# Optimization experiments

Measured on AMD Instinct MI355X. Metric: run time of the kernel, lower is better.

## Reference

```python
import jax, jax.numpy as jnp
import numpy as np

T = 0.07
TOPK = 5

def _l2norm(x, axis=-1, eps=1e-12):
    n = jnp.sqrt(jnp.sum(x * x, axis=axis, keepdims=True))
    return x / jnp.maximum(n, eps)

def setup_inputs() -> dict:
    key = jax.random.key(0)
    k1, k2, k3, k4, k5 = jax.random.split(key, 5)
    b, nc, dim, dim_mlp, K = 256, 5, 128, 2048, 65536
    q = jax.random.normal(k1, (b, nc, dim), jnp.float32)
    k = jax.random.normal(k2, (b, dim), jnp.float32)
    q_backbone = jax.random.normal(k3, (b, nc, dim_mlp), jnp.float32)
    # queues are column-normalized buffers, as in __init__
    queue = _l2norm(jax.random.normal(k4, (dim, K), jnp.float32), axis=0)
    queue_backbone = _l2norm(jax.random.normal(k5, (dim_mlp, K), jnp.float32), axis=0)
    return {"q": q, "k": k, "q_backbone": q_backbone,
            "queue": queue, "queue_backbone": queue_backbone}

def reference(q, k, q_backbone, queue, queue_backbone):
    b, nc, dim = q.shape
    dim_mlp = q_backbone.shape[-1]
    qn = _l2norm(q)                 # [b, nc, dim]
    kn = _l2norm(k)                 # [b, dim]
    qb = _l2norm(q_backbone)        # [b, nc, dim_mlp]

    # positive logits: each crop vs its key
    l_pos = jnp.einsum('bnd,bd->bn', qn, kn).reshape(-1, 1)      # [b*nc, 1]
    # negative logits vs queue
    l_neg = jnp.einsum('nc,ck->nk', qn.reshape(-1, dim), queue)  # [b*nc, K]
    logits = jnp.concatenate([l_pos, l_neg], axis=1) / T
    labels = jnp.zeros((logits.shape[0],), dtype=jnp.int32)

    # backbone-space similarities to pick top-k neighbors
    l_neg_backbone = jnp.einsum('nc,ck->nk', qb.reshape(-1, dim_mlp), queue_backbone)

    # pull_topk: softmax CE pulling toward top-k backbone neighbors.
    # scatter-mask + masked mean == gather log-softmax at top-k indices (indices distinct)
    _, knn_idx = jax.lax.top_k(l_neg_backbone, TOPK)             # [b*nc, TOPK]
    log_prob = jax.nn.log_softmax(l_neg / T, axis=1)             # [b*nc, K]
    pos_logp = jnp.take_along_axis(log_prob, knn_idx, axis=1)    # [b*nc, TOPK]
    loss = -jnp.mean(jnp.mean(pos_logp, axis=1))
    return logits, labels, loss
```

## Files before the change

### kernel.cpp

```cpp
#include <hip/hip_runtime.h>
#include <hip/hip_bf16.h>

#define M_     1280
#define DIM    128
#define DMLP   2048
#define KQ     65536
#define NCOLS  65537ull
#define NTOPK  5
#define NCHUNK 256
#define NBLK1  512
#define NTK    32
#define INV_T  14.285714285714286f

typedef __attribute__((ext_vector_type(8))) short bf16x8;
typedef __attribute__((ext_vector_type(4))) float f32x4;

static __device__ __forceinline__ unsigned short f2bf(float x){
  union { __hip_bfloat16 h; unsigned short u; } cv;
  cv.h = __float2bfloat16(x);
  return cv.u;
}

#define GLDS16(gp, lp) __builtin_amdgcn_global_load_lds( \
    (const __attribute__((address_space(1))) void*)(gp), \
    (__attribute__((address_space(3))) void*)(lp), 16, 0, 0)

#define BAR()   asm volatile("s_barrier" ::: "memory")
#define VMW(n)  asm volatile("s_waitcnt vmcnt(" #n ")" ::: "memory")

__global__ __launch_bounds__(256) void transpose_bf16(
    const float* __restrict__ in, unsigned short* __restrict__ out, int R, int C){
  __shared__ float tile[64][65];
  const int c0 = blockIdx.x * 64, r0 = blockIdx.y * 64;
  const int t = threadIdx.x;
  #pragma unroll
  for (int i = 0; i < 4; ++i){
    int lin = t + i * 256;
    int rr = lin >> 4;
    int cc = (lin & 15) * 4;
    const float4 v = *(const float4*)(in + (size_t)(r0 + rr) * C + c0 + cc);
    tile[rr][cc + 0] = v.x; tile[rr][cc + 1] = v.y;
    tile[rr][cc + 2] = v.z; tile[rr][cc + 3] = v.w;
  }
  __syncthreads();
  #pragma unroll
  for (int i = 0; i < 4; ++i){
    int lin = t + i * 256;
    int oc  = lin >> 4;
    int orr = (lin & 15) * 4;
    ushort4 u;
    u.x = f2bf(tile[orr + 0][oc]); u.y = f2bf(tile[orr + 1][oc]);
    u.z = f2bf(tile[orr + 2][oc]); u.w = f2bf(tile[orr + 3][oc]);
    *(ushort4*)(out + (size_t)(c0 + oc) * R + r0 + orr) = u;
  }
}

__global__ __launch_bounds__(128) void normq_kernel(
    const float* __restrict__ q, const float* __restrict__ k,
    unsigned short* __restrict__ qn, float* __restrict__ outp){
  const int i = blockIdx.x;
  const int t = threadIdx.x;
  const float qv = q[(size_t)i * DIM + t];
  const float kv = k[(size_t)(i / 5) * DIM + t];
  float a = qv * qv, b = kv * kv, d = qv * kv;
  #pragma unroll
  for (int s = 32; s >= 1; s >>= 1){
    a += __shfl_down(a, s, 64);
    b += __shfl_down(b, s, 64);
    d += __shfl_down(d, s, 64);
  }
  __shared__ float red[6];
  if ((t & 63) == 0){ red[(t >> 6) * 3 + 0] = a; red[(t >> 6) * 3 + 1] = b; red[(t >> 6) * 3 + 2] = d; }
  __syncthreads();
  const float qq = red[0] + red[3], kk = red[1] + red[4], qk = red[2] + red[5];
  const float qnorm = fmaxf(sqrtf(qq), 1e-12f);
  qn[(size_t)i * DIM + t] = f2bf(qv / qnorm);
  if (t == 0){
    const float knorm = fmaxf(sqrtf(kk), 1e-12f);
    outp[(size_t)i * NCOLS] = (qk / (qnorm * knorm)) * INV_T;
  }
}

__global__ __launch_bounds__(256) void normqb_kernel(
    const float* __restrict__ qb, unsigned short* __restrict__ out){
  const int i = blockIdx.x, t = threadIdx.x;
  const float* p = qb + (size_t)i * DMLP;
  float x[8]; float ss = 0.f;
  #pragma unroll
  for (int j = 0; j < 8; ++j){ x[j] = p[t + j * 256]; ss += x[j] * x[j]; }
  #pragma unroll
  for (int s = 32; s >= 1; s >>= 1) ss += __shfl_down(ss, s, 64);
  __shared__ float r4[4];
  if ((t & 63) == 0) r4[t >> 6] = ss;
  __syncthreads();
  const float tot = r4[0] + r4[1] + r4[2] + r4[3];
  const float inv = 1.0f / fmaxf(sqrtf(tot), 1e-12f);
  unsigned short* o = out + (size_t)i * DMLP;
  #pragma unroll
  for (int j = 0; j < 8; ++j) o[t + j * 256] = f2bf(x[j] * inv);
}

static __device__ __forceinline__ void tk_insert(float* v, int* ix, float nv, int ni){
  if (nv > v[4]){
    v[4] = nv; ix[4] = ni;
    #pragma unroll
    for (int j = 4; j > 0; --j){
      if (v[j] > v[j - 1]){
        float tv = v[j]; v[j] = v[j - 1]; v[j - 1] = tv;
        int   ti = ix[j]; ix[j] = ix[j - 1]; ix[j - 1] = ti;
      }
    }
  }
}

__global__ __launch_bounds__(256) void gemm1_mfma(
    const unsigned short* __restrict__ A, const unsigned short* __restrict__ BT,
    float* __restrict__ outp, float* __restrict__ pm, float* __restrict__ ps){
  __shared__ __attribute__((aligned(16))) unsigned char smem[16512];
  unsigned short* At = (unsigned short*)smem;
  unsigned short* Bt = At + 128 * 32;

  const int t    = threadIdx.x;
  const int lane = t & 63;
  const int wv   = t >> 6;
  const int lid  = lane & 15;
  const int quad = lane >> 4;
  const int m0 = blockIdx.x * 128;
  const int n0 = blockIdx.y * 128;

  f32x4 acc[2][8];
  #pragma unroll
  for (int mt = 0; mt < 2; ++mt)
    #pragma unroll
    for (int nt = 0; nt < 8; ++nt)
      acc[mt][nt] = f32x4{0.f, 0.f, 0.f, 0.f};

  const int arow = t >> 2;
  const int ace  = (t & 3) * 8;

  for (int kt = 0; kt < DIM; kt += 32){
    if (kt) __syncthreads();
    #pragma unroll
    for (int it = 0; it < 2; ++it){
      int row = arow + it * 64;
      GLDS16(A  + (size_t)(m0 + row) * DIM + kt + ace, At + (t + it * 256) * 8);
    }
    #pragma unroll
    for (int it = 0; it < 2; ++it){
      int row = arow + it * 64;
      GLDS16(BT + (size_t)(n0 + row) * DIM + kt + ace, Bt + (t + it * 256) * 8);
    }
    asm volatile("s_waitcnt vmcnt(0)" ::: "memory");
    __syncthreads();

    bf16x8 af[2], bfr[8];
    #pragma unroll
    for (int mt = 0; mt < 2; ++mt)
      af[mt] = *(const bf16x8*)(At + (wv * 32 + mt * 16 + lid) * 32 + quad * 8);
    #pragma unroll
    for (int nt = 0; nt < 8; ++nt)
      bfr[nt] = *(const bf16x8*)(Bt + (nt * 16 + lid) * 32 + quad * 8);
    #pragma unroll
    for (int mt = 0; mt < 2; ++mt)
      #pragma unroll
      for (int nt = 0; nt < 8; ++nt)
        acc[mt][nt] = __builtin_amdgcn_mfma_f32_16x16x32_bf16(af[mt], bfr[nt], acc[mt][nt], 0, 0, 0);
  }

  float mx[2][4], sm[2][4];
  #pragma unroll
  for (int mt = 0; mt < 2; ++mt)
    #pragma unroll
    for (int r = 0; r < 4; ++r) mx[mt][r] = -3.0e38f;
  #pragma unroll
  for (int mt = 0; mt < 2; ++mt)
    #pragma unroll
    for (int nt = 0; nt < 8; ++nt)
      #pragma unroll
      for (int r = 0; r < 4; ++r){
        const int mg = m0 + wv * 32 + mt * 16 + quad * 4 + r;
        const int ng = n0 + nt * 16 + lid;
        const float x = acc[mt][nt][r] * INV_T;
        outp[(size_t)mg * NCOLS + 1 + ng] = x;
        mx[mt][r] = fmaxf(mx[mt][r], x);
      }
  #pragma unroll
  for (int mt = 0; mt < 2; ++mt)
    #pragma unroll
    for (int r = 0; r < 4; ++r){
      #pragma unroll
      for (int s = 8; s >= 1; s >>= 1)
        mx[mt][r] = fmaxf(mx[mt][r], __shfl_xor(mx[mt][r], s, 64));
      sm[mt][r] = 0.f;
    }
  #pragma unroll
  for (int mt = 0; mt < 2; ++mt)
    #pragma unroll
    for (int nt = 0; nt < 8; ++nt)
      #pragma unroll
      for (int r = 0; r < 4; ++r)
        sm[mt][r] += __expf(acc[mt][nt][r] * INV_T - mx[mt][r]);
  #pragma unroll
  for (int mt = 0; mt < 2; ++mt)
    #pragma unroll
    for (int r = 0; r < 4; ++r){
      #pragma unroll
      for (int s = 8; s >= 1; s >>= 1)
        sm[mt][r] += __shfl_xor(sm[mt][r], s, 64);
      if (lid == 0){
        const int mg = m0 + wv * 32 + mt * 16 + quad * 4 + r;
        pm[(size_t)mg * NBLK1 + blockIdx.y] = mx[mt][r];
        ps[(size_t)mg * NBLK1 + blockIdx.y] = sm[mt][r];
      }
    }
}


static __device__ __forceinline__ void stage_half_g2_dummy(){}

#define RDA(mi_, SRC) do { _Pragma("unroll") for (int mf = 0; mf < 4; ++mf){ \
    const int R_ = (mi_) * 128 + wm * 64 + mf * 16 + lid; \
    av[mi_][mf][0] = *(const bf16x8*)((SRC) + R_ * 64 + sw0); \
    av[mi_][mf][1] = *(const bf16x8*)((SRC) + R_ * 64 + sw1); } } while(0)

#define RDB(nj_, SRC) do { _Pragma("unroll") for (int nf = 0; nf < 2; ++nf){ \
    const int S_ = (nj_) * 128 + wn * 32 + nf * 16 + lid; \
    bv[nj_][nf][0] = *(const bf16x8*)((SRC) + S_ * 64 + sw0); \
    bv[nj_][nf][1] = *(const bf16x8*)((SRC) + S_ * 64 + sw1); } } while(0)

#define MMQ(mi_, nj_) do { __builtin_amdgcn_s_setprio(1); \
    _Pragma("unroll") for (int mf = 0; mf < 4; ++mf) \
    _Pragma("unroll") for (int nf = 0; nf < 2; ++nf){ \
      acc[mi_][nj_][mf][nf] = __builtin_amdgcn_mfma_f32_16x16x32_bf16(av[mi_][mf][0], bv[nj_][nf][0], acc[mi_][nj_][mf][nf], 0, 0, 0); \
      acc[mi_][nj_][mf][nf] = __builtin_amdgcn_mfma_f32_16x16x32_bf16(av[mi_][mf][1], bv[nj_][nf][1], acc[mi_][nj_][mf][nf], 0, 0, 0); } \
    __builtin_amdgcn_s_setprio(0); } while(0)

#define STAGE(base, kc, dst) do { \
  GLDS16((base) + ro0 + (kc), (dst) + t * 8); \
  GLDS16((base) + ro1 + (kc), (dst) + (512 + t) * 8); } while(0)

__global__ __launch_bounds__(512, 2) void gemm2_topk(
    const unsigned short* __restrict__ A, const unsigned short* __restrict__ BT,
    float* __restrict__ cval, int* __restrict__ cidx){
  __shared__ __attribute__((aligned(16))) unsigned short lds[2][2][256 * 64];

  const int t    = threadIdx.x;
  const int lane = t & 63;
  const int wv   = t >> 6;
  const int wm   = wv >> 2;
  const int wn   = wv & 3;
  const int lid  = lane & 15;
  const int quad = lane >> 4;
  const int l7   = lid & 7;
  const int sw0  = ((quad    ) ^ l7) * 8;
  const int sw1  = ((quad ^ 4) ^ l7) * 8;

  const int h  = blockIdx.x;
  const int wg = (h & 7) * 160 + (h >> 3);
  const int bm = wg % 5;
  const int bn = wg / 5;
  const int m0 = bm * 256;
  const int n0 = bn * 256;

  const int r0s = t >> 3,        r1s = (512 + t) >> 3;
  const int g0  = (t & 7) ^ (r0s & 7), g1 = (t & 7) ^ (r1s & 7);
  const int ro0 = r0s * DMLP + g0 * 8;
  const int ro1 = r1s * DMLP + g1 * 8;
  const unsigned short* aB0 = A  + (size_t)m0          * DMLP;
  const unsigned short* aB1 = A  + (size_t)(m0 + 128)  * DMLP;
  const unsigned short* bB0 = BT + (size_t)n0          * DMLP;
  const unsigned short* bB1 = BT + (size_t)(n0 + 128)  * DMLP;

  f32x4 acc[2][2][4][2];
  #pragma unroll
  for (int a = 0; a < 2; ++a)
    #pragma unroll
    for (int b = 0; b < 2; ++b)
      #pragma unroll
      for (int c = 0; c < 4; ++c)
        #pragma unroll
        for (int d = 0; d < 2; ++d)
          acc[a][b][c][d] = f32x4{0.f, 0.f, 0.f, 0.f};

  bf16x8 av[2][4][2];
  bf16x8 bv[2][2][2];

  STAGE(aB0, 0, &lds[0][0][0]);
  STAGE(bB0, 0, &lds[0][1][0]);
  STAGE(aB1, 0, &lds[0][0][128 * 64]);
  STAGE(bB1, 0, &lds[0][1][128 * 64]);
  VMW(0);
  BAR();

  #pragma unroll 2
  for (int kt = 0; kt < NTK; ++kt){
    unsigned short* curA = &lds[kt & 1][0][0];
    unsigned short* curB = &lds[kt & 1][1][0];
    unsigned short* nxtA = &lds[(kt + 1) & 1][0][0];
    unsigned short* nxtB = &lds[(kt + 1) & 1][1][0];

    if (kt) MMQ(0, 1);

    RDA(0, curA);
    RDB(0, curB);

    if (kt + 1 < NTK){
      const int kc = (kt + 1) * 64;
      STAGE(aB0, kc, nxtA);
      STAGE(bB0, kc, nxtB);
      STAGE(aB1, kc, nxtA + 128 * 64);
      STAGE(bB1, kc, nxtB + 128 * 64);
    }

    MMQ(0, 0);
    RDA(1, curA);
    MMQ(1, 0);
    RDB(1, curB);
    MMQ(1, 1);

    VMW(0);
    BAR();
  }
  MMQ(0, 1);

  float* scratch = (float*)&lds[0][0][0];
  const int erow = t >> 2;
  const int eh   = t & 3;
  #pragma unroll
  for (int mi = 0; mi < 2; ++mi){
    float v[5]; int ix[5];
    #pragma unroll
    for (int j = 0; j < 5; ++j){ v[j] = -3.0e38f; ix[j] = 0; }
    #pragma unroll
    for (int nj = 0; nj < 2; ++nj){
      __syncthreads();
      #pragma unroll
      for (int mf = 0; mf < 4; ++mf)
        #pragma unroll
        for (int nf = 0; nf < 2; ++nf)
          #pragma unroll
          for (int r = 0; r < 4; ++r)
            scratch[(wm * 64 + mf * 16 + quad * 4 + r) * 133 + wn * 32 + nf * 16 + lid]
              = acc[mi][nj][mf][nf][r];
      __syncthreads();
      for (int j = 0; j < 32; ++j)
        tk_insert(v, ix, scratch[erow * 133 + j * 4 + eh], n0 + nj * 128 + j * 4 + eh);
    }
    #pragma unroll
    for (int s = 1; s <= 2; s <<= 1){
      float pv[5]; int pi[5];
      #pragma unroll
      for (int j = 0; j < 5; ++j){ pv[j] = __shfl_xor(v[j], s, 64); pi[j] = __shfl_xor(ix[j], s, 64); }
      #pragma unroll
      for (int j = 0; j < 5; ++j) tk_insert(v, ix, pv[j], pi[j]);
    }
    if (eh == 0){
      const int rowg = m0 + mi * 128 + erow;
      const size_t cb = ((size_t)rowg * NCHUNK + bn) * NTOPK;
      #pragma unroll
      for (int j = 0; j < 5; ++j){ cval[cb + j] = v[j]; cidx[cb + j] = ix[j]; }
    }
  }
}

__global__ __launch_bounds__(256) void topk_merge(
    const float* __restrict__ cval, const int* __restrict__ cidx, int* __restrict__ knn){
  const int row = blockIdx.x, t = threadIdx.x;
  float v[5]; int ix[5];
  #pragma unroll
  for (int j = 0; j < 5; ++j){ v[j] = -3.0e38f; ix[j] = 0; }
  const size_t base = (size_t)row * (NCHUNK * NTOPK);
  #pragma unroll
  for (int j = 0; j < 5; ++j){
    const int c = t * 5 + j;
    tk_insert(v, ix, cval[base + c], cidx[base + c]);
  }
  __shared__ float lv[256 * 5];
  __shared__ int   li[256 * 5];
  #pragma unroll
  for (int j = 0; j < 5; ++j){ lv[t * 5 + j] = v[j]; li[t * 5 + j] = ix[j]; }
  __syncthreads();
  if (t < 64){
    float v2[5]; int ix2[5];
    #pragma unroll
    for (int j = 0; j < 5; ++j){ v2[j] = -3.0e38f; ix2[j] = 0; }
    for (int L = 0; L < 4; ++L)
      #pragma unroll
      for (int j = 0; j < 5; ++j)
        tk_insert(v2, ix2, lv[(t * 4 + L) * 5 + j], li[(t * 4 + L) * 5 + j]);
    #pragma unroll
    for (int s = 32; s >= 1; s >>= 1){
      float pv[5]; int pi[5];
      #pragma unroll
      for (int j = 0; j < 5; ++j){ pv[j] = __shfl_down(v2[j], s, 64); pi[j] = __shfl_down(ix2[j], s, 64); }
      #pragma unroll
      for (int j = 0; j < 5; ++j) tk_insert(v2, ix2, pv[j], pi[j]);
    }
    if (t == 0){
      #pragma unroll
      for (int j = 0; j < 5; ++j) knn[(size_t)row * NTOPK + j] = ix2[j];
    }
  }
}

__global__ __launch_bounds__(256) void lse_merge(
    const float* __restrict__ pm, const float* __restrict__ ps,
    float* __restrict__ lse){
  const int row = blockIdx.x, t = threadIdx.x;
  const float* pmr = pm + (size_t)row * NBLK1;
  const float* psr = ps + (size_t)row * NBLK1;
  float m = -1.0e30f, s = 0.f;
  #pragma unroll
  for (int c = 0; c < 2; ++c){
    const float om = pmr[t + c * 256], os = psr[t + c * 256];
    const float nm = fmaxf(m, om);
    s = s * __expf(m - nm) + os * __expf(om - nm);
    m = nm;
  }
  #pragma unroll
  for (int sh = 32; sh >= 1; sh >>= 1){
    const float om = __shfl_down(m, sh, 64), os = __shfl_down(s, sh, 64);
    const float nm = fmaxf(m, om);
    s = s * __expf(m - nm) + os * __expf(om - nm);
    m = nm;
  }
  __shared__ float sm2[4], ss2[4];
  if ((t & 63) == 0){ sm2[t >> 6] = m; ss2[t >> 6] = s; }
  __syncthreads();
  if (t == 0){
    float M = sm2[0], S = ss2[0];
    #pragma unroll
    for (int w = 1; w < 4; ++w){
      const float nm = fmaxf(M, sm2[w]);
      S = S * __expf(M - nm) + ss2[w] * __expf(sm2[w] - nm);
      M = nm;
    }
    lse[row] = M + __logf(S);
  }
}

__global__ __launch_bounds__(256) void loss_kernel(
    const float* __restrict__ logits, const float* __restrict__ lse,
    const int* __restrict__ knn, float* __restrict__ loss){
  const int i = blockIdx.x * 256 + threadIdx.x;
  float c = 0.f;
  if (i < M_){
    const float l = lse[i];
    #pragma unroll
    for (int j = 0; j < 5; ++j){
      const int id = knn[(size_t)i * NTOPK + j];
      c += l - logits[(size_t)i * NCOLS + 1 + id];
    }
    c *= (1.0f / 6400.0f);
  }
  #pragma unroll
  for (int s = 32; s >= 1; s >>= 1) c += __shfl_down(c, s, 64);
  if ((threadIdx.x & 63) == 0) atomicAdd(loss, c);
}

extern "C" void kernel_launch(void* const* d_in, const int* in_sizes, int n_in,
                              void* d_out, int out_size, void* d_ws, size_t ws_size,
                              hipStream_t stream){
  const float* q   = (const float*)d_in[0];
  const float* k   = (const float*)d_in[1];
  const float* qbI = (const float*)d_in[2];
  const float* que = (const float*)d_in[3];
  const float* qbb = (const float*)d_in[4];
  float* out = (float*)d_out;

  unsigned char* w = (unsigned char*)d_ws;
  unsigned short* qn   = (unsigned short*)w; w += (size_t)M_ * DIM  * 2;
  unsigned short* qbn  = (unsigned short*)w; w += (size_t)M_ * DMLP * 2;
  unsigned short* queT = (unsigned short*)w; w += (size_t)KQ * DIM  * 2;
  unsigned short* qbbT = (unsigned short*)w; w += (size_t)KQ * DMLP * 2;
  float* cval = (float*)w;                   w += (size_t)M_ * NCHUNK * NTOPK * 4;
  int*   cidx = (int*)w;                     w += (size_t)M_ * NCHUNK * NTOPK * 4;
  int*   knn  = (int*)w;                     w += (size_t)M_ * NTOPK * 4;
  float* lseb = (float*)w;                   w += (size_t)M_ * 4;
  float* pm   = (float*)w;                   w += (size_t)M_ * NBLK1 * 4;
  float* ps   = (float*)w;                   w += (size_t)M_ * NBLK1 * 4;

  hipMemsetAsync(out + (size_t)M_ * NCOLS, 0, (M_ + 1) * sizeof(float), stream);

  transpose_bf16<<<dim3(KQ / 64, DIM  / 64), 256, 0, stream>>>(que, queT, DIM,  KQ);
  transpose_bf16<<<dim3(KQ / 64, DMLP / 64), 256, 0, stream>>>(qbb, qbbT, DMLP, KQ);
  normq_kernel <<<M_, 128, 0, stream>>>(q, k, qn, out);
  normqb_kernel<<<M_, 256, 0, stream>>>(qbI, qbn);
  gemm1_mfma<<<dim3(10, NBLK1), 256, 0, stream>>>(qn, queT, out, pm, ps);
  gemm2_topk<<<dim3(1280), 512, 0, stream>>>(qbn, qbbT, cval, cidx);
  topk_merge<<<M_, 256, 0, stream>>>(cval, cidx, knn);
  lse_merge<<<M_, 256, 0, stream>>>(pm, ps, lseb);
  loss_kernel<<<(M_ + 255) / 256, 256, 0, stream>>>(out, lseb, knn,
                                                    out + (size_t)M_ * NCOLS + M_);
}
```

Before: 1.386 ms.

## Run backbone top-k GEMM in FP8 e4m3 with a repacked LDS layout

The backbone queue transpose and the normalized backbone queries are now quantized to FP8 e4m3 instead of bf16. The top-k GEMM kernel is rewritten around 16x16x32 fp8 MFMA, with a new swizzled 64-byte-row LDS layout and a smaller shared buffer so launch bounds allow 4 blocks per CU. This halves global and LDS bytes for the largest GEMM and the transpose writes. The cost is much coarser precision: normalized 2048-d vectors have entries near the e4m3 subnormal range, so the top-5 neighbor indices may differ from the reference.

```diff
diff --git a/kernel.cpp b/kernel.cpp
--- a/kernel.cpp
+++ b/kernel.cpp
@@ -1,5 +1,6 @@
 #include <hip/hip_runtime.h>
 #include <hip/hip_bf16.h>
+#include <hip/hip_fp8.h>
 
 #define M_     1280
 #define DIM    128
@@ -21,6 +22,11 @@
   return cv.u;
 }
 
+static __device__ __forceinline__ unsigned char f2f8(float x){
+  __hip_fp8_e4m3 h(x);
+  return (unsigned char)h.__x;
+}
+
 #define GLDS16(gp, lp) __builtin_amdgcn_global_load_lds( \
     (const __attribute__((address_space(1))) void*)(gp), \
     (__attribute__((address_space(3))) void*)(lp), 16, 0, 0)
@@ -52,6 +58,33 @@
     u.x = f2bf(tile[orr + 0][oc]); u.y = f2bf(tile[orr + 1][oc]);
     u.z = f2bf(tile[orr + 2][oc]); u.w = f2bf(tile[orr + 3][oc]);
     *(ushort4*)(out + (size_t)(c0 + oc) * R + r0 + orr) = u;
+  }
+}
+
+__global__ __launch_bounds__(256) void transpose_fp8(
+    const float* __restrict__ in, unsigned char* __restrict__ out, int R, int C){
+  __shared__ float tile[64][65];
+  const int c0 = blockIdx.x * 64, r0 = blockIdx.y * 64;
+  const int t = threadIdx.x;
+  #pragma unroll
+  for (int i = 0; i < 4; ++i){
+    int lin = t + i * 256;
+    int rr = lin >> 4;
+    int cc = (lin & 15) * 4;
+    const float4 v = *(const float4*)(in + (size_t)(r0 + rr) * C + c0 + cc);
+    tile[rr][cc + 0] = v.x; tile[rr][cc + 1] = v.y;
+    tile[rr][cc + 2] = v.z; tile[rr][cc + 3] = v.w;
+  }
+  __syncthreads();
+  #pragma unroll
+  for (int i = 0; i < 4; ++i){
+    int lin = t + i * 256;
+    int oc  = lin >> 4;
+    int orr = (lin & 15) * 4;
+    uchar4 u;
+    u.x = f2f8(tile[orr + 0][oc]); u.y = f2f8(tile[orr + 1][oc]);
+    u.z = f2f8(tile[orr + 2][oc]); u.w = f2f8(tile[orr + 3][oc]);
+    *(uchar4*)(out + (size_t)(c0 + oc) * R + r0 + orr) = u;
   }
 }
 
@@ -82,7 +115,7 @@
 }
 
 __global__ __launch_bounds__(256) void normqb_kernel(
-    const float* __restrict__ qb, unsigned short* __restrict__ out){
+    const float* __restrict__ qb, unsigned char* __restrict__ out){
   const int i = blockIdx.x, t = threadIdx.x;
   const float* p = qb + (size_t)i * DMLP;
   float x[8]; float ss = 0.f;
@@ -95,9 +128,9 @@
   __syncthreads();
   const float tot = r4[0] + r4[1] + r4[2] + r4[3];
   const float inv = 1.0f / fmaxf(sqrtf(tot), 1e-12f);
-  unsigned short* o = out + (size_t)i * DMLP;
-  #pragma unroll
-  for (int j = 0; j < 8; ++j) o[t + j * 256] = f2bf(x[j] * inv);
+  unsigned char* o = out + (size_t)i * DMLP;
+  #pragma unroll
+  for (int j = 0; j < 8; ++j) o[t + j * 256] = f2f8(x[j] * inv);
 }
 
 static __device__ __forceinline__ void tk_insert(float* v, int* ix, float nv, int ni){
@@ -216,33 +249,29 @@
 }
 
 
-static __device__ __forceinline__ void stage_half_g2_dummy(){}
-
-#define RDA(mi_, SRC) do { _Pragma("unroll") for (int mf = 0; mf < 4; ++mf){ \
-    const int R_ = (mi_) * 128 + wm * 64 + mf * 16 + lid; \
-    av[mi_][mf][0] = *(const bf16x8*)((SRC) + R_ * 64 + sw0); \
-    av[mi_][mf][1] = *(const bf16x8*)((SRC) + R_ * 64 + sw1); } } while(0)
-
-#define RDB(nj_, SRC) do { _Pragma("unroll") for (int nf = 0; nf < 2; ++nf){ \
-    const int S_ = (nj_) * 128 + wn * 32 + nf * 16 + lid; \
-    bv[nj_][nf][0] = *(const bf16x8*)((SRC) + S_ * 64 + sw0); \
-    bv[nj_][nf][1] = *(const bf16x8*)((SRC) + S_ * 64 + sw1); } } while(0)
-
-#define MMQ(mi_, nj_) do { __builtin_amdgcn_s_setprio(1); \
+#define RDA8(mi_, SRC) do { _Pragma("unroll") for (int mf = 0; mf < 4; ++mf){ \
+    const int rr = ((mi_) * 64 + wm * 32 + mf * 8 + r2l) * 128; \
+    av[mi_][mf][0] = *(const long*)((SRC) + rr + c0f); \
+    av[mi_][mf][1] = *(const long*)((SRC) + rr + c1f); } } while(0)
+
+#define RDB8(nj_, SRC) do { _Pragma("unroll") for (int nf = 0; nf < 2; ++nf){ \
+    const int rr = ((nj_) * 64 + wn * 16 + nf * 8 + r2l) * 128; \
+    bv[nf][0] = *(const long*)((SRC) + rr + c0f); \
+    bv[nf][1] = *(const long*)((SRC) + rr + c1f); } } while(0)
+
+#define MMQ8(mi_, nj_) do { __builtin_amdgcn_s_setprio(1); \
     _Pragma("unroll") for (int mf = 0; mf < 4; ++mf) \
     _Pragma("unroll") for (int nf = 0; nf < 2; ++nf){ \
-      acc[mi_][nj_][mf][nf] = __builtin_amdgcn_mfma_f32_16x16x32_bf16(av[mi_][mf][0], bv[nj_][nf][0], acc[mi_][nj_][mf][nf], 0, 0, 0); \
-      acc[mi_][nj_][mf][nf] = __builtin_amdgcn_mfma_f32_16x16x32_bf16(av[mi_][mf][1], bv[nj_][nf][1], acc[mi_][nj_][mf][nf], 0, 0, 0); } \
+      acc[mi_][nj_][mf][nf] = __builtin_amdgcn_mfma_f32_16x16x32_fp8_fp8(av[mi_][mf][0], bv[nf][0], acc[mi_][nj_][mf][nf], 0, 0, 0); \
+      acc[mi_][nj_][mf][nf] = __builtin_amdgcn_mfma_f32_16x16x32_fp8_fp8(av[mi_][mf][1], bv[nf][1], acc[mi_][nj_][mf][nf], 0, 0, 0); } \
     __builtin_amdgcn_s_setprio(0); } while(0)
 
-#define STAGE(base, kc, dst) do { \
-  GLDS16((base) + ro0 + (kc), (dst) + t * 8); \
-  GLDS16((base) + ro1 + (kc), (dst) + (512 + t) * 8); } while(0)
-
-__global__ __launch_bounds__(512, 2) void gemm2_topk(
-    const unsigned short* __restrict__ A, const unsigned short* __restrict__ BT,
+#define STAGE8(base, kc, dst) GLDS16((base) + roff + (kc), (dst) + (size_t)t * 16)
+
+__global__ __launch_bounds__(512, 4) void gemm2_topk(
+    const unsigned char* __restrict__ A, const unsigned char* __restrict__ BT,
     float* __restrict__ cval, int* __restrict__ cidx){
-  __shared__ __attribute__((aligned(16))) unsigned short lds[2][2][256 * 64];
+  __shared__ __attribute__((aligned(16))) unsigned char smem[66048];
 
   const int t    = threadIdx.x;
   const int lane = t & 63;
@@ -251,9 +280,9 @@
   const int wn   = wv & 3;
   const int lid  = lane & 15;
   const int quad = lane >> 4;
-  const int l7   = lid & 7;
-  const int sw0  = ((quad    ) ^ l7) * 8;
-  const int sw1  = ((quad ^ 4) ^ l7) * 8;
+  const int r2l  = lid >> 1;
+  const int c0f = ((((lid & 1) * 4 + 0 + (quad >> 1)) ^ r2l) * 16) + (quad & 1) * 8;
+  const int c1f = ((((lid & 1) * 4 + 2 + (quad >> 1)) ^ r2l) * 16) + (quad & 1) * 8;
 
   const int h  = blockIdx.x;
   const int wg = (h & 7) * 160 + (h >> 3);
@@ -262,14 +291,15 @@
   const int m0 = bm * 256;
   const int n0 = bn * 256;
 
-  const int r0s = t >> 3,        r1s = (512 + t) >> 3;
-  const int g0  = (t & 7) ^ (r0s & 7), g1 = (t & 7) ^ (r1s & 7);
-  const int ro0 = r0s * DMLP + g0 * 8;
-  const int ro1 = r1s * DMLP + g1 * 8;
-  const unsigned short* aB0 = A  + (size_t)m0          * DMLP;
-  const unsigned short* aB1 = A  + (size_t)(m0 + 128)  * DMLP;
-  const unsigned short* bB0 = BT + (size_t)n0          * DMLP;
-  const unsigned short* bB1 = BT + (size_t)(n0 + 128)  * DMLP;
+  const int p     = t;
+  const int r2loc = p >> 3;
+  const int u     = (p & 7) ^ (r2loc & 7);
+  const int rloc  = r2loc * 2 + (u >> 2);
+  const size_t roff = (size_t)rloc * DMLP + (u & 3) * 16;
+  const unsigned char* aB0 = A  + (size_t)m0 * DMLP;
+  const unsigned char* aB1 = A  + (size_t)(m0 + 128) * DMLP;
+  const unsigned char* bB0 = BT + (size_t)n0 * DMLP;
+  const unsigned char* bB1 = BT + (size_t)(n0 + 128) * DMLP;
 
   f32x4 acc[2][2][4][2];
   #pragma unroll
@@ -282,48 +312,48 @@
         for (int d = 0; d < 2; ++d)
           acc[a][b][c][d] = f32x4{0.f, 0.f, 0.f, 0.f};
 
-  bf16x8 av[2][4][2];
-  bf16x8 bv[2][2][2];
-
-  STAGE(aB0, 0, &lds[0][0][0]);
-  STAGE(bB0, 0, &lds[0][1][0]);
-  STAGE(aB1, 0, &lds[0][0][128 * 64]);
-  STAGE(bB1, 0, &lds[0][1][128 * 64]);
+  long av[2][4][2];
+  long bv[2][2];
+
+  STAGE8(aB0, 0, smem);
+  STAGE8(bB0, 0, smem + 16384);
+  STAGE8(aB1, 0, smem + 8192);
+  STAGE8(bB1, 0, smem + 16384 + 8192);
   VMW(0);
   BAR();
 
   #pragma unroll 2
   for (int kt = 0; kt < NTK; ++kt){
-    unsigned short* curA = &lds[kt & 1][0][0];
-    unsigned short* curB = &lds[kt & 1][1][0];
-    unsigned short* nxtA = &lds[(kt + 1) & 1][0][0];
-    unsigned short* nxtB = &lds[(kt + 1) & 1][1][0];
-
-    if (kt) MMQ(0, 1);
-
-    RDA(0, curA);
-    RDB(0, curB);
+    unsigned char* curA = smem + (kt & 1) * 32768;
+    unsigned char* curB = curA + 16384;
+    unsigned char* nxtA = smem + ((kt + 1) & 1) * 32768;
+    unsigned char* nxtB = nxtA + 16384;
+
+    if (kt) MMQ8(0, 1);
+
+    RDA8(0, curA);
+    RDB8(0, curB);
 
     if (kt + 1 < NTK){
       const int kc = (kt + 1) * 64;
-      STAGE(aB0, kc, nxtA);
-      STAGE(bB0, kc, nxtB);
-      STAGE(aB1, kc, nxtA + 128 * 64);
-      STAGE(bB1, kc, nxtB + 128 * 64);
-    }
-
-    MMQ(0, 0);
-    RDA(1, curA);
-    MMQ(1, 0);
-    RDB(1, curB);
-    MMQ(1, 1);
+      STAGE8(aB0, kc, nxtA);
+      STAGE8(bB0, kc, nxtB);
+      STAGE8(aB1, kc, nxtA + 8192);
+      STAGE8(bB1, kc, nxtB + 8192);
+    }
+
+    MMQ8(0, 0);
+    RDA8(1, curA);
+    MMQ8(1, 0);
+    RDB8(1, curB);
+    MMQ8(1, 1);
 
     VMW(0);
     BAR();
   }
-  MMQ(0, 1);
-
-  float* scratch = (float*)&lds[0][0][0];
+  MMQ8(0, 1);
+
+  float* scratch = (float*)smem;
   const int erow = t >> 2;
   const int eh   = t & 3;
   #pragma unroll
@@ -340,11 +370,11 @@
         for (int nf = 0; nf < 2; ++nf)
           #pragma unroll
           for (int r = 0; r < 4; ++r)
-            scratch[(wm * 64 + mf * 16 + quad * 4 + r) * 133 + wn * 32 + nf * 16 + lid]
+            scratch[(wm * 64 + mf * 16 + quad * 4 + r) * 129 + wn * 32 + nf * 16 + lid]
               = acc[mi][nj][mf][nf][r];
       __syncthreads();
       for (int j = 0; j < 32; ++j)
-        tk_insert(v, ix, scratch[erow * 133 + j * 4 + eh], n0 + nj * 128 + j * 4 + eh);
+        tk_insert(v, ix, scratch[erow * 129 + j * 4 + eh], n0 + nj * 128 + j * 4 + eh);
     }
     #pragma unroll
     for (int s = 1; s <= 2; s <<= 1){
@@ -469,25 +499,25 @@
   float* out = (float*)d_out;
 
   unsigned char* w = (unsigned char*)d_ws;
-  unsigned short* qn   = (unsigned short*)w; w += (size_t)M_ * DIM  * 2;
-  unsigned short* qbn  = (unsigned short*)w; w += (size_t)M_ * DMLP * 2;
-  unsigned short* queT = (unsigned short*)w; w += (size_t)KQ * DIM  * 2;
-  unsigned short* qbbT = (unsigned short*)w; w += (size_t)KQ * DMLP * 2;
-  float* cval = (float*)w;                   w += (size_t)M_ * NCHUNK * NTOPK * 4;
-  int*   cidx = (int*)w;                     w += (size_t)M_ * NCHUNK * NTOPK * 4;
-  int*   knn  = (int*)w;                     w += (size_t)M_ * NTOPK * 4;
-  float* lseb = (float*)w;                   w += (size_t)M_ * 4;
-  float* pm   = (float*)w;                   w += (size_t)M_ * NBLK1 * 4;
-  float* ps   = (float*)w;                   w += (size_t)M_ * NBLK1 * 4;
+  unsigned short* qn    = (unsigned short*)w; w += (size_t)M_ * DIM  * 2;
+  unsigned char*  qbn8  = (unsigned char*)w;  w += (size_t)M_ * DMLP;
+  unsigned short* queT  = (unsigned short*)w; w += (size_t)KQ * DIM  * 2;
+  unsigned char*  qbbT8 = (unsigned char*)w;  w += (size_t)KQ * DMLP;
+  float* cval = (float*)w;                    w += (size_t)M_ * NCHUNK * NTOPK * 4;
+  int*   cidx = (int*)w;                      w += (size_t)M_ * NCHUNK * NTOPK * 4;
+  int*   knn  = (int*)w;                      w += (size_t)M_ * NTOPK * 4;
+  float* lseb = (float*)w;                    w += (size_t)M_ * 4;
+  float* pm   = (float*)w;                    w += (size_t)M_ * NBLK1 * 4;
+  float* ps   = (float*)w;                    w += (size_t)M_ * NBLK1 * 4;
 
   hipMemsetAsync(out + (size_t)M_ * NCOLS, 0, (M_ + 1) * sizeof(float), stream);
 
-  transpose_bf16<<<dim3(KQ / 64, DIM  / 64), 256, 0, stream>>>(que, queT, DIM,  KQ);
-  transpose_bf16<<<dim3(KQ / 64, DMLP / 64), 256, 0, stream>>>(qbb, qbbT, DMLP, KQ);
+  transpose_bf16<<<dim3(KQ / 64, DIM  / 64), 256, 0, stream>>>(que, queT, DIM, KQ);
+  transpose_fp8 <<<dim3(KQ / 64, DMLP / 64), 256, 0, stream>>>(qbb, qbbT8, DMLP, KQ);
   normq_kernel <<<M_, 128, 0, stream>>>(q, k, qn, out);
-  normqb_kernel<<<M_, 256, 0, stream>>>(qbI, qbn);
+  normqb_kernel<<<M_, 256, 0, stream>>>(qbI, qbn8);
   gemm1_mfma<<<dim3(10, NBLK1), 256, 0, stream>>>(qn, queT, out, pm, ps);
-  gemm2_topk<<<dim3(1280), 512, 0, stream>>>(qbn, qbbT, cval, cidx);
+  gemm2_topk<<<dim3(1280), 512, 0, stream>>>(qbn8, qbbT8, cval, cidx);
   topk_merge<<<M_, 256, 0, stream>>>(cval, cidx, knn);
   lse_merge<<<M_, 256, 0, stream>>>(pm, ps, lseb);
   loss_kernel<<<(M_ + 255) / 256, 256, 0, stream>>>(out, lseb, knn,
```

Result: slower. 2.749 ms (+98.3%).
